# Kernel tuning notes

Measured on AMD Instinct MI355X. Metric: run time of the kernel, lower is better.

## Reference

```python
import jax, jax.numpy as jnp
import numpy as np

BN_EPS = 1e-5
N_NODES = 100000
N_EDGES = 1600000
F_IN = 128
F_HID = 256
N_ITEMS = 128


def setup_inputs() -> dict:
    key = jax.random.key(0)
    ks = jax.random.split(key, 6)
    return {
        "node_feature": jax.random.normal(ks[0], (N_NODES, F_IN), jnp.float32),
        "edge_index": jax.random.randint(ks[1], (2, N_EDGES), 0, N_NODES, jnp.int64),
        "items_ready_to_cache": jnp.arange(N_ITEMS, dtype=jnp.int64),
        "gcn_w": jax.random.normal(ks[2], (F_IN, F_HID), jnp.float32) / np.sqrt(F_IN),
        "gcn_b": jnp.zeros((F_HID,), jnp.float32),
        "bn_gamma": jnp.ones((F_HID,), jnp.float32),
        "bn_beta": jnp.zeros((F_HID,), jnp.float32),
        "emb_table": jax.random.normal(ks[3], (F_IN, F_IN), jnp.float32),
        "proj_w": jax.random.normal(ks[4], (F_HID, F_IN), jnp.float32) / np.sqrt(F_HID),
        "proj_b": jnp.zeros((F_IN,), jnp.float32),
    }


def _gcn_conv(x, edge_index, w, b, n_nodes):
    # PyG GCNConv: add self-loops, symmetric normalization, scatter-add to target.
    loop = jnp.arange(n_nodes, dtype=edge_index.dtype)
    src = jnp.concatenate([edge_index[0], loop])
    dst = jnp.concatenate([edge_index[1], loop])
    h = x @ w                                  # [N, F_HID]
    deg = jax.ops.segment_sum(jnp.ones_like(dst, dtype=h.dtype), dst,
                              num_segments=n_nodes)
    dinv = jnp.where(deg > 0, jax.lax.rsqrt(deg), 0.0)
    norm = dinv[src] * dinv[dst]               # [E+N]
    msgs = h[src] * norm[:, None]              # gather + scale  [E+N, F_HID]
    out = jax.ops.segment_sum(msgs, dst, num_segments=n_nodes)  # scatter-add
    return out + b


def reference(node_feature, edge_index, items_ready_to_cache, gcn_w, gcn_b,
              bn_gamma, bn_beta, emb_table, proj_w, proj_b):
    n_nodes = node_feature.shape[0]
    x = _gcn_conv(node_feature, edge_index, gcn_w, gcn_b, n_nodes)
    # BatchNorm1d in training mode: batch stats (biased variance)
    mean = jnp.mean(x, axis=0)
    var = jnp.mean((x - mean) ** 2, axis=0)
    x = bn_gamma * (x - mean) * jax.lax.rsqrt(var + BN_EPS) + bn_beta
    x = jax.nn.relu(x)
    rsu_embedding = x[0:1] @ proj_w + proj_b   # [1, F_IN]
    # item_id_to_index collapses indices to arange(len(items))
    n_items = items_ready_to_cache.shape[0]
    items_embeddings = emb_table[jnp.arange(n_items)]  # [n_items, F_IN]
    scores = items_embeddings @ rsu_embedding[0]       # [n_items]
    return scores, rsu_embedding
```

## Files before the change

### kernel.cpp

```cpp
#include <hip/hip_runtime.h>
#include <hip/hip_bf16.h>


#define THREADS 256

__global__ __launch_bounds__(THREADS) void deg_rank_kernel(const int* __restrict__ ei,
                                                           int* __restrict__ deg,
                                                           int* __restrict__ rank,
                                                           int E, int N) {
    int e4 = (blockIdx.x * THREADS + threadIdx.x) * 4;
    if (e4 + 3 < E) {
        int4 d = *(const int4*)(ei + E + e4);
        int4 r;
        r.x = ((unsigned)d.x < (unsigned)N) ? atomicAdd(&deg[d.x], 1) : 0;
        r.y = ((unsigned)d.y < (unsigned)N) ? atomicAdd(&deg[d.y], 1) : 0;
        r.z = ((unsigned)d.z < (unsigned)N) ? atomicAdd(&deg[d.z], 1) : 0;
        r.w = ((unsigned)d.w < (unsigned)N) ? atomicAdd(&deg[d.w], 1) : 0;
        *(int4*)(rank + e4) = r;
    } else if (e4 < E) {
        for (int u = e4; u < E; ++u) {
            unsigned d = (unsigned)ei[E + u];
            rank[u] = (d < (unsigned)N) ? atomicAdd(&deg[d], 1) : 0;
        }
    }
}

__global__ __launch_bounds__(THREADS) void scan_kernel(const int* __restrict__ deg,
                                                       int* __restrict__ rowptr,
                                                       int* __restrict__ bsum,
                                                       int* __restrict__ boff,
                                                       float* __restrict__ dinv,
                                                       int* __restrict__ ctr, int n) {
    __shared__ int sh[THREADS];
    __shared__ int isLast;
    const int t = threadIdx.x, b = blockIdx.x;
    const int base = b * 1024 + t * 4;
    int v0 = (base + 0 < n) ? deg[base + 0] : 0;
    int v1 = (base + 1 < n) ? deg[base + 1] : 0;
    int v2 = (base + 2 < n) ? deg[base + 2] : 0;
    int v3 = (base + 3 < n) ? deg[base + 3] : 0;
    if (base + 0 < n) dinv[base + 0] = rsqrtf((float)(v0 + 1));
    if (base + 1 < n) dinv[base + 1] = rsqrtf((float)(v1 + 1));
    if (base + 2 < n) dinv[base + 2] = rsqrtf((float)(v2 + 1));
    if (base + 3 < n) dinv[base + 3] = rsqrtf((float)(v3 + 1));
    const int local = v0 + v1 + v2 + v3;
    sh[t] = local;
    __syncthreads();
    int run = local;
    for (int off = 1; off < THREADS; off <<= 1) {
        int add = (t >= off) ? sh[t - off] : 0;
        __syncthreads();
        run += add;
        sh[t] = run;
        __syncthreads();
    }
    const int excl = run - local;
    if (base + 0 < n) rowptr[base + 0] = excl;
    if (base + 1 < n) rowptr[base + 1] = excl + v0;
    if (base + 2 < n) rowptr[base + 2] = excl + v0 + v1;
    if (base + 3 < n) rowptr[base + 3] = excl + v0 + v1 + v2;
    if (t == 0) {
        bsum[b] = sh[THREADS - 1];
        __threadfence();
        isLast = (atomicAdd(ctr, 1) == (int)gridDim.x - 1);
    }
    __syncthreads();
    if (isLast) {
        __threadfence();
        const int nb = gridDim.x;
        const int lv = (t < nb) ? bsum[t] : 0;
        sh[t] = lv;
        __syncthreads();
        int r2 = lv;
        for (int off = 1; off < THREADS; off <<= 1) {
            int add = (t >= off) ? sh[t - off] : 0;
            __syncthreads();
            r2 += add;
            sh[t] = r2;
            __syncthreads();
        }
        boff[t] = r2 - lv;
    }
}

__global__ __launch_bounds__(THREADS) void scatter_kernel(const int* __restrict__ ei,
                                                          const int* __restrict__ rowptr,
                                                          const int* __restrict__ boff,
                                                          const int* __restrict__ rank,
                                                          int* __restrict__ csr,
                                                          int E, int N) {
    int e4 = (blockIdx.x * THREADS + threadIdx.x) * 4;
    if (e4 + 3 < E) {
        int4 d = *(const int4*)(ei + E + e4);
        int4 s = *(const int4*)(ei + e4);
        int4 r = *(const int4*)(rank + e4);
        if ((unsigned)d.x < (unsigned)N) {
            int p = rowptr[d.x] + boff[d.x >> 10] + r.x;
            if ((unsigned)p < (unsigned)E) csr[p] = s.x;
        }
        if ((unsigned)d.y < (unsigned)N) {
            int p = rowptr[d.y] + boff[d.y >> 10] + r.y;
            if ((unsigned)p < (unsigned)E) csr[p] = s.y;
        }
        if ((unsigned)d.z < (unsigned)N) {
            int p = rowptr[d.z] + boff[d.z >> 10] + r.z;
            if ((unsigned)p < (unsigned)E) csr[p] = s.z;
        }
        if ((unsigned)d.w < (unsigned)N) {
            int p = rowptr[d.w] + boff[d.w >> 10] + r.w;
            if ((unsigned)p < (unsigned)E) csr[p] = s.w;
        }
    } else if (e4 < E) {
        for (int u = e4; u < E; ++u) {
            unsigned d = (unsigned)ei[E + u];
            if (d < (unsigned)N) {
                int p = rowptr[d] + boff[d >> 10] + rank[u];
                if ((unsigned)p < (unsigned)E) csr[p] = ei[u];
            }
        }
    }
}

__global__ __launch_bounds__(THREADS) void agg_kernel(const float* __restrict__ x,
                                                      const int* __restrict__ rowptr,
                                                      const int* __restrict__ boff,
                                                      const int* __restrict__ csr,
                                                      const float* __restrict__ dinv,
                                                      float* __restrict__ agg,
                                                      int n, int E) {
    const int lane = threadIdx.x & 63;
    const int wid  = blockIdx.x * (THREADS >> 6) + (threadIdx.x >> 6);
    const int nw   = gridDim.x * (THREADS >> 6);
    const float* xl = x + lane * 2;
    for (int i = wid; i < n; i += nw) {
        const int e0 = rowptr[i] + boff[i >> 10];
        const int e1 = (i + 1 < n) ? rowptr[i + 1] + boff[(i + 1) >> 10] : E;
        const float di = dinv[i];
        const float2 xs = *(const float2*)(xl + (size_t)i * 128);
        float ax = di * xs.x, ay = di * xs.y;
        int e = e0;
        for (; e + 8 <= e1; e += 8) {
            int ss[8]; float ww[8]; float2 pv[8];
#pragma unroll
            for (int u = 0; u < 8; ++u) {
                int s = csr[e + u];
                ss[u] = ((unsigned)s < (unsigned)n) ? s : 0;
            }
#pragma unroll
            for (int u = 0; u < 8; ++u) ww[u] = dinv[ss[u]];
#pragma unroll
            for (int u = 0; u < 8; ++u)
                pv[u] = *(const float2*)(xl + (size_t)ss[u] * 128);
#pragma unroll
            for (int u = 0; u < 8; ++u) {
                ax = fmaf(ww[u], pv[u].x, ax);
                ay = fmaf(ww[u], pv[u].y, ay);
            }
        }
        for (; e < e1; ++e) {
            int s = csr[e];
            s = ((unsigned)s < (unsigned)n) ? s : 0;
            float w = dinv[s];
            float2 p = *(const float2*)(xl + (size_t)s * 128);
            ax = fmaf(w, p.x, ax);
            ay = fmaf(w, p.y, ay);
        }
        *(float2*)(agg + (size_t)i * 128 + lane * 2) = make_float2(di * ax, di * ay);
    }
}

__global__ __launch_bounds__(512) void syrk_kernel(const float* __restrict__ agg,
                                                   float* __restrict__ G,
                                                   float* __restrict__ colsumS,
                                                   int n, int NCHK) {
    __shared__ float Asm[32 * 132];
    const int t = threadIdx.x;
    const int p0 = (t >> 5) * 8;
    const int q0 = (t & 31) * 4;
    float acc[8][4];
#pragma unroll
    for (int i = 0; i < 8; ++i)
#pragma unroll
        for (int j = 0; j < 4; ++j) acc[i][j] = 0.f;
    float s_acc = 0.f;

    for (int c = blockIdx.x; c < NCHK; c += gridDim.x) {
#pragma unroll
        for (int u = 0; u < 2; ++u) {
            int f4 = t * 2 + u;
            int r = f4 >> 5, c4 = f4 & 31;
            int gr = c * 32 + r;
            float4 v = make_float4(0.f, 0.f, 0.f, 0.f);
            if (gr < n) v = *(const float4*)(agg + (size_t)gr * 128 + c4 * 4);
            *(float4*)(Asm + r * 132 + c4 * 4) = v;
        }
        __syncthreads();
#pragma unroll 4
        for (int r = 0; r < 32; ++r) {
            const float* row = Asm + r * 132;
            float4 a0 = *(const float4*)(row + p0);
            float4 a1 = *(const float4*)(row + p0 + 4);
            float4 bq = *(const float4*)(row + q0);
            float ap[8] = {a0.x, a0.y, a0.z, a0.w, a1.x, a1.y, a1.z, a1.w};
            float aq[4] = {bq.x, bq.y, bq.z, bq.w};
#pragma unroll
            for (int pp = 0; pp < 8; ++pp)
#pragma unroll
                for (int qq = 0; qq < 4; ++qq)
                    acc[pp][qq] = fmaf(ap[pp], aq[qq], acc[pp][qq]);
        }
        if (t < 128) {
            float sa = 0.f;
#pragma unroll 4
            for (int r = 0; r < 32; ++r) sa += Asm[r * 132 + t];
            s_acc += sa;
        }
        __syncthreads();
    }
#pragma unroll
    for (int pp = 0; pp < 8; ++pp) {
        atomicAdd(&G[(p0 + pp) * 128 + q0 + 0], acc[pp][0]);
        atomicAdd(&G[(p0 + pp) * 128 + q0 + 1], acc[pp][1]);
        atomicAdd(&G[(p0 + pp) * 128 + q0 + 2], acc[pp][2]);
        atomicAdd(&G[(p0 + pp) * 128 + q0 + 3], acc[pp][3]);
    }
    if (t < 128) atomicAdd(&colsumS[t], s_acc);
}

__global__ __launch_bounds__(THREADS) void stats_fin_kernel(
        const float* __restrict__ G, const float* __restrict__ W,
        const float* __restrict__ bias, const float* __restrict__ colsumS,
        const float* __restrict__ agg, float* __restrict__ colsum,
        float* __restrict__ colsumsq, float* __restrict__ row0,
        const float* __restrict__ gamma, const float* __restrict__ beta,
        const float* __restrict__ proj_w, const float* __restrict__ proj_b,
        const float* __restrict__ emb, float* __restrict__ out,
        int* __restrict__ ctr, int n, int n_items) {
    __shared__ float wsm[128];
    __shared__ float red[THREADS], red2[THREADS], red3[THREADS];
    __shared__ int isLast;
    const int t = threadIdx.x, j = blockIdx.x;
    if (t < 128) wsm[t] = W[t * 256 + j];
    __syncthreads();
    float part = 0.f;
    const float wq = wsm[t & 127];
    const int pbase = t >> 7;
#pragma unroll 8
    for (int u = 0; u < 64; ++u)
        part = fmaf(G[u * 256 + t], wsm[pbase + u * 2], part);
    red[t] = part * wq;
    red2[t] = (t < 128) ? colsumS[t] * wsm[t] : 0.f;
    red3[t] = (t < 128) ? agg[t] * wsm[t] : 0.f;
    __syncthreads();
    for (int s = 128; s > 0; s >>= 1) {
        if (t < s) { red[t] += red[t + s]; red2[t] += red2[t + s]; red3[t] += red3[t + s]; }
        __syncthreads();
    }
    if (t == 0) {
        const float b = bias[j];
        const float sw = red2[0];
        colsum[j]   = sw + (float)n * b;
        colsumsq[j] = red[0] + 2.f * b * sw + (float)n * b * b;
        row0[j]     = red3[0] + b;
        __threadfence();
        isLast = (atomicAdd(ctr, 1) == (int)gridDim.x - 1);
    }
    __syncthreads();
    if (!isLast) return;
    __threadfence();
    __shared__ float x0[256];
    __shared__ float rsu[128];
    const float invn = 1.0f / (float)n;
    {
        float mean = colsum[t] * invn;
        float var = colsumsq[t] * invn - mean * mean;
        float r = rsqrtf(var + 1e-5f);
        float v = gamma[t] * (row0[t] - mean) * r + beta[t];
        x0[t] = v > 0.f ? v : 0.f;
    }
    __syncthreads();
    if (t < 128) {
        float sacc = proj_b[t];
        for (int c = 0; c < 256; ++c) sacc = fmaf(x0[c], proj_w[c * 128 + t], sacc);
        rsu[t] = sacc;
        out[128 + t] = sacc;
    }
    __syncthreads();
    if (t < n_items) {
        float sacc = 0.f;
        for (int jj = 0; jj < 128; ++jj) sacc = fmaf(emb[t * 128 + jj], rsu[jj], sacc);
        out[t] = sacc;
    }
}

extern "C" void kernel_launch(void* const* d_in, const int* in_sizes, int n_in,
                              void* d_out, int out_size, void* d_ws, size_t ws_size,
                              hipStream_t stream) {
    const float* node_feature = (const float*)d_in[0];
    const int*   edge_index   = (const int*)d_in[1];
    const float* gcn_w  = (const float*)d_in[3];
    const float* gcn_b  = (const float*)d_in[4];
    const float* bn_g   = (const float*)d_in[5];
    const float* bn_b   = (const float*)d_in[6];
    const float* emb    = (const float*)d_in[7];
    const float* proj_w = (const float*)d_in[8];
    const float* proj_b = (const float*)d_in[9];
    float* out = (float*)d_out;

    const int N = in_sizes[0] / 128;
    const int E = in_sizes[1] / 2;
    const int n_items = in_sizes[2];

    char* base = (char*)d_ws;
    size_t off = 0;
    auto alloc = [&](size_t bytes) -> void* {
        void* p = (void*)(base + off);
        off += (bytes + 255) & ~(size_t)255;
        return p;
    };
    int*   deg      = (int*)alloc((size_t)N * 4);
    float* G        = (float*)alloc(16384 * 4);
    float* colsumS  = (float*)alloc(128 * 4);
    int*   ctrs     = (int*)alloc(256);
    const size_t zero_bytes = off;
    int*   rank     = (int*)alloc((size_t)E * 4);
    int*   rowptr   = (int*)alloc((size_t)N * 4);
    int*   bsum     = (int*)alloc(256 * 4);
    int*   boff     = (int*)alloc(256 * 4);
    float* dinv     = (float*)alloc((size_t)N * 4);
    int*   csr      = (int*)alloc((size_t)E * 4);
    float* colsum   = (float*)alloc(256 * 4);
    float* colsumsq = (float*)alloc(256 * 4);
    float* row0     = (float*)alloc(256 * 4);
    float* agg      = (float*)alloc((size_t)N * 128 * 4);
    (void)ws_size;

    const int nbE4 = (E / 4 + THREADS - 1) / THREADS;
    const int nchunks = (N + 1023) >> 10;
    const int NCHK = (N + 31) / 32;

    hipMemsetAsync(deg, 0, zero_bytes, stream);

    deg_rank_kernel<<<nbE4, THREADS, 0, stream>>>(edge_index, deg, rank, E, N);
    scan_kernel<<<nchunks, THREADS, 0, stream>>>(deg, rowptr, bsum, boff, dinv,
                                                 &ctrs[0], N);
    scatter_kernel<<<nbE4, THREADS, 0, stream>>>(edge_index, rowptr, boff, rank,
                                                 csr, E, N);
    agg_kernel<<<2048, THREADS, 0, stream>>>(node_feature, rowptr, boff, csr, dinv,
                                             agg, N, E);
    syrk_kernel<<<512, 512, 0, stream>>>(agg, G, colsumS, N, NCHK);
    stats_fin_kernel<<<256, THREADS, 0, stream>>>(G, gcn_w, gcn_b, colsumS, agg,
                                                  colsum, colsumsq, row0, bn_g, bn_b,
                                                  proj_w, proj_b, emb, out,
                                                  &ctrs[1], N, n_items);
}
```

Before: 524.0 us.

## Use nontemporal loads/stores, split aggregation launch, and reduce syrk partials without atomics

```diff
diff --git a/kernel.cpp b/kernel.cpp
--- a/kernel.cpp
+++ b/kernel.cpp
@@ -3,6 +3,26 @@
 
 
 #define THREADS 256
+
+typedef int   i32x4 __attribute__((ext_vector_type(4)));
+typedef float f32x4 __attribute__((ext_vector_type(4)));
+
+static __device__ __forceinline__ int4 ntload_i4(const int* p) {
+    i32x4 v = __builtin_nontemporal_load((const i32x4*)p);
+    return make_int4(v.x, v.y, v.z, v.w);
+}
+static __device__ __forceinline__ float4 ntload_f4(const float* p) {
+    f32x4 v = __builtin_nontemporal_load((const f32x4*)p);
+    return make_float4(v.x, v.y, v.z, v.w);
+}
+static __device__ __forceinline__ void ntstore_i4(int* p, int4 v) {
+    i32x4 t = {v.x, v.y, v.z, v.w};
+    __builtin_nontemporal_store(t, (i32x4*)p);
+}
+static __device__ __forceinline__ void ntstore_f4(float* p, float4 v) {
+    f32x4 t = {v.x, v.y, v.z, v.w};
+    __builtin_nontemporal_store(t, (f32x4*)p);
+}
 
 __global__ __launch_bounds__(THREADS) void deg_rank_kernel(const int* __restrict__ ei,
                                                            int* __restrict__ deg,
@@ -10,13 +30,13 @@
                                                            int E, int N) {
     int e4 = (blockIdx.x * THREADS + threadIdx.x) * 4;
     if (e4 + 3 < E) {
-        int4 d = *(const int4*)(ei + E + e4);
+        int4 d = ntload_i4(ei + E + e4);
         int4 r;
         r.x = ((unsigned)d.x < (unsigned)N) ? atomicAdd(&deg[d.x], 1) : 0;
         r.y = ((unsigned)d.y < (unsigned)N) ? atomicAdd(&deg[d.y], 1) : 0;
         r.z = ((unsigned)d.z < (unsigned)N) ? atomicAdd(&deg[d.z], 1) : 0;
         r.w = ((unsigned)d.w < (unsigned)N) ? atomicAdd(&deg[d.w], 1) : 0;
-        *(int4*)(rank + e4) = r;
+        ntstore_i4(rank + e4, r);
     } else if (e4 < E) {
         for (int u = e4; u < E; ++u) {
             unsigned d = (unsigned)ei[E + u];
@@ -91,9 +111,9 @@
                                                           int E, int N) {
     int e4 = (blockIdx.x * THREADS + threadIdx.x) * 4;
     if (e4 + 3 < E) {
-        int4 d = *(const int4*)(ei + E + e4);
-        int4 s = *(const int4*)(ei + e4);
-        int4 r = *(const int4*)(rank + e4);
+        int4 d = ntload_i4(ei + E + e4);
+        int4 s = ntload_i4(ei + e4);
+        int4 r = ntload_i4(rank + e4);
         if ((unsigned)d.x < (unsigned)N) {
             int p = rowptr[d.x] + boff[d.x >> 10] + r.x;
             if ((unsigned)p < (unsigned)E) csr[p] = s.x;
@@ -127,12 +147,12 @@
                                                       const int* __restrict__ csr,
                                                       const float* __restrict__ dinv,
                                                       float* __restrict__ agg,
-                                                      int n, int E) {
+                                                      int rb, int re, int n, int E) {
     const int lane = threadIdx.x & 63;
     const int wid  = blockIdx.x * (THREADS >> 6) + (threadIdx.x >> 6);
     const int nw   = gridDim.x * (THREADS >> 6);
     const float* xl = x + lane * 2;
-    for (int i = wid; i < n; i += nw) {
+    for (int i = rb + wid; i < re; i += nw) {
         const int e0 = rowptr[i] + boff[i >> 10];
         const int e1 = (i + 1 < n) ? rowptr[i + 1] + boff[(i + 1) >> 10] : E;
         const float di = dinv[i];
@@ -143,7 +163,7 @@
             int ss[8]; float ww[8]; float2 pv[8];
 #pragma unroll
             for (int u = 0; u < 8; ++u) {
-                int s = csr[e + u];
+                int s = __builtin_nontemporal_load(csr + e + u);
                 ss[u] = ((unsigned)s < (unsigned)n) ? s : 0;
             }
 #pragma unroll
@@ -158,19 +178,21 @@
             }
         }
         for (; e < e1; ++e) {
-            int s = csr[e];
+            int s = __builtin_nontemporal_load(csr + e);
             s = ((unsigned)s < (unsigned)n) ? s : 0;
             float w = dinv[s];
             float2 p = *(const float2*)(xl + (size_t)s * 128);
             ax = fmaf(w, p.x, ax);
             ay = fmaf(w, p.y, ay);
         }
-        *(float2*)(agg + (size_t)i * 128 + lane * 2) = make_float2(di * ax, di * ay);
+        float2 o = make_float2(di * ax, di * ay);
+        __builtin_nontemporal_store(*(double*)&o,
+                                    (double*)(agg + (size_t)i * 128 + lane * 2));
     }
 }
 
 __global__ __launch_bounds__(512) void syrk_kernel(const float* __restrict__ agg,
-                                                   float* __restrict__ G,
+                                                   float* __restrict__ Gpart,
                                                    float* __restrict__ colsumS,
                                                    int n, int NCHK) {
     __shared__ float Asm[32 * 132];
@@ -191,7 +213,7 @@
             int r = f4 >> 5, c4 = f4 & 31;
             int gr = c * 32 + r;
             float4 v = make_float4(0.f, 0.f, 0.f, 0.f);
-            if (gr < n) v = *(const float4*)(agg + (size_t)gr * 128 + c4 * 4);
+            if (gr < n) v = ntload_f4(agg + (size_t)gr * 128 + c4 * 4);
             *(float4*)(Asm + r * 132 + c4 * 4) = v;
         }
         __syncthreads();
@@ -217,14 +239,28 @@
         }
         __syncthreads();
     }
-#pragma unroll
-    for (int pp = 0; pp < 8; ++pp) {
-        atomicAdd(&G[(p0 + pp) * 128 + q0 + 0], acc[pp][0]);
-        atomicAdd(&G[(p0 + pp) * 128 + q0 + 1], acc[pp][1]);
-        atomicAdd(&G[(p0 + pp) * 128 + q0 + 2], acc[pp][2]);
-        atomicAdd(&G[(p0 + pp) * 128 + q0 + 3], acc[pp][3]);
-    }
+    float* gp = Gpart + (size_t)blockIdx.x * 16384;
+#pragma unroll
+    for (int pp = 0; pp < 8; ++pp)
+        ntstore_f4(gp + (p0 + pp) * 128 + q0,
+                   make_float4(acc[pp][0], acc[pp][1], acc[pp][2], acc[pp][3]));
     if (t < 128) atomicAdd(&colsumS[t], s_acc);
+}
+
+__global__ __launch_bounds__(THREADS) void greduce_kernel(const float* __restrict__ Gpart,
+                                                          float* __restrict__ G, int NB) {
+    const int seg = blockIdx.x >> 4;
+    const int i4 = (blockIdx.x & 15) * THREADS + threadIdx.x;
+    const int b0 = (seg * NB) / 8, b1 = ((seg + 1) * NB) / 8;
+    float4 a = make_float4(0.f, 0.f, 0.f, 0.f);
+    for (int b = b0; b < b1; ++b) {
+        float4 v = ntload_f4(Gpart + (size_t)b * 16384 + i4 * 4);
+        a.x += v.x; a.y += v.y; a.z += v.z; a.w += v.w;
+    }
+    atomicAdd(&G[i4 * 4 + 0], a.x);
+    atomicAdd(&G[i4 * 4 + 1], a.y);
+    atomicAdd(&G[i4 * 4 + 2], a.z);
+    atomicAdd(&G[i4 * 4 + 3], a.w);
 }
 
 __global__ __launch_bounds__(THREADS) void stats_fin_kernel(
@@ -333,11 +369,15 @@
     float* colsumsq = (float*)alloc(256 * 4);
     float* row0     = (float*)alloc(256 * 4);
     float* agg      = (float*)alloc((size_t)N * 128 * 4);
-    (void)ws_size;
+    int NB = (int)((ws_size > off) ? ((ws_size - off) / 65536) : 0);
+    if (NB > 512) NB = 512;
+    if (NB < 8) NB = 8;
+    float* Gpart    = (float*)alloc((size_t)NB * 16384 * 4);
 
     const int nbE4 = (E / 4 + THREADS - 1) / THREADS;
     const int nchunks = (N + 1023) >> 10;
     const int NCHK = (N + 31) / 32;
+    const int N2 = N / 2;
 
     hipMemsetAsync(deg, 0, zero_bytes, stream);
 
@@ -347,8 +387,11 @@
     scatter_kernel<<<nbE4, THREADS, 0, stream>>>(edge_index, rowptr, boff, rank,
                                                  csr, E, N);
     agg_kernel<<<2048, THREADS, 0, stream>>>(node_feature, rowptr, boff, csr, dinv,
-                                             agg, N, E);
-    syrk_kernel<<<512, 512, 0, stream>>>(agg, G, colsumS, N, NCHK);
+                                             agg, 0, N2, N, E);
+    agg_kernel<<<2048, THREADS, 0, stream>>>(node_feature, rowptr, boff, csr, dinv,
+                                             agg, N2, N, N, E);
+    syrk_kernel<<<NB, 512, 0, stream>>>(agg, Gpart, colsumS, N, NCHK);
+    greduce_kernel<<<128, THREADS, 0, stream>>>(Gpart, G, NB);
     stats_fin_kernel<<<256, THREADS, 0, stream>>>(G, gcn_w, gcn_b, colsumS, agg,
                                                   colsum, colsumsq, row0, bn_g, bn_b,
                                                   proj_w, proj_b, emb, out,
```

New measurement: 454.8 us. 1.15x faster.
